# Optimization experiments

Measured on AMD Instinct MI355X. Metric: run time of the kernel, lower is better.

## Reference

```python
import jax, jax.numpy as jnp
import numpy as np

BATCH = 8192
IN_DIM = 2048
OUT_DIM = 2048
DEPTH = 5


def setup_inputs() -> dict:
    key = jax.random.key(0)
    k1, k2, k3, k4 = jax.random.split(key, 4)
    x = jax.random.normal(k1, (BATCH, IN_DIM), dtype=jnp.float32)
    hyperdimensional_weights = jax.random.normal(k2, (DEPTH, IN_DIM, OUT_DIM), dtype=jnp.float32)
    classical_weights = jax.random.normal(k3, (IN_DIM, OUT_DIM), dtype=jnp.float32)
    classical_biases = jax.random.normal(k4, (OUT_DIM,), dtype=jnp.float32)
    return {
        "x": x,
        "hyperdimensional_weights": hyperdimensional_weights,
        "classical_weights": classical_weights,
        "classical_biases": classical_biases,
    }


def _hyperdimensional_probs(hd_w):
    # angle = W[d, j, 0], phase = W[d, j, 1] for output index j (j < input_dims)
    depth, in_dim, _ = hd_w.shape
    angles = hd_w[:, :OUT_DIM, 0]   # [depth, out]
    phases = hd_w[:, :OUT_DIM, 1]   # [depth, out]
    # Initial uniform state 1/sqrt(n), replicated per output unit j.
    s0 = jnp.full((OUT_DIM, in_dim), 1.0 / np.sqrt(in_dim), dtype=jnp.complex64)

    def step(s, ang_ph):
        ang, ph = ang_ph                      # each [out]
        c = jnp.cos(ang)[:, None]
        sn = jnp.sin(ang)[:, None]
        # Circulant rotation: new[k] = cos*s[k] - sin*s[k+1] + sin*s[k-1] (cyclic)
        s = c * s - sn * jnp.roll(s, -1, axis=1) + sn * jnp.roll(s, 1, axis=1)
        # Global phase gate: diag(e^{i*phase})
        s = s * jnp.exp(1j * ph)[:, None]
        return s, None

    s, _ = jax.lax.scan(step, s0, (angles, phases))
    # probability = |state[0]|^2
    return jnp.abs(s[:, 0]) ** 2              # [out], real float32


def reference(x, hyperdimensional_weights, classical_weights, classical_biases):
    classical = x @ classical_weights + classical_biases            # [B, out]
    hd = _hyperdimensional_probs(hyperdimensional_weights)          # [out] (batch-independent)
    return jnp.tanh(classical + hd[None, :])
```

## Files before the change

kernel.cpp:

```cpp
#include <hip/hip_runtime.h>

#define BATCH 8192
#define DIM   2048
#define DEPTH 5


#define BUFSZ  65536
#define ABYTES 32768

typedef short bf16x8_t __attribute__((ext_vector_type(8)));
typedef float f32x4_t  __attribute__((ext_vector_type(4)));

__device__ __forceinline__ unsigned short f2bf(float f) {
  unsigned u = __float_as_uint(f);
  u += 0x7fffu + ((u >> 16) & 1u);
  return (unsigned short)(u >> 16);
}
__device__ __forceinline__ float bf2f(unsigned short h) {
  return __uint_as_float(((unsigned)h) << 16);
}

__global__ void prep_fused_kernel(const float* __restrict__ x,
                                  const float* __restrict__ hdw,
                                  const float* __restrict__ W,
                                  const float* __restrict__ bias,
                                  float* __restrict__ bias2,
                                  unsigned short* __restrict__ xhi,
                                  unsigned short* __restrict__ xlo,
                                  unsigned short* __restrict__ whi,
                                  unsigned short* __restrict__ wlo) {
  __shared__ float tile[32][33];
  const int b = blockIdx.x;
  const int tid = threadIdx.x;

  if (b < 8192) {
    size_t g = (size_t)b * 256 + tid;
    const float4* xp = (const float4*)(x + g * 8);
    float4 v0 = xp[0], v1 = xp[1];
    float v[8] = {v0.x, v0.y, v0.z, v0.w, v1.x, v1.y, v1.z, v1.w};
    bf16x8_t h, lo;
#pragma unroll
    for (int j = 0; j < 8; ++j) {
      unsigned short hj = f2bf(v[j]);
      h[j] = (short)hj;
      lo[j] = (short)f2bf(v[j] - bf2f(hj));
    }
    ((bf16x8_t*)xhi)[g] = h;
    ((bf16x8_t*)xlo)[g] = lo;
  } else if (b < 12288) {
    const int t = b - 8192;
    const int k0 = (t >> 6) * 32;
    const int n0 = (t & 63) * 32;
    const int tx = tid & 31;
    const int ty = tid >> 5;
#pragma unroll
    for (int r = 0; r < 32; r += 8)
      tile[ty + r][tx] = W[(size_t)(k0 + ty + r) * DIM + n0 + tx];
    __syncthreads();
    const int n = tid >> 3;
    const int kq = (tid & 7) * 4;
    ushort4 hv, lv;
    float vv0 = tile[kq + 0][n], vv1 = tile[kq + 1][n];
    float vv2 = tile[kq + 2][n], vv3 = tile[kq + 3][n];
    hv.x = f2bf(vv0); lv.x = f2bf(vv0 - bf2f(hv.x));
    hv.y = f2bf(vv1); lv.y = f2bf(vv1 - bf2f(hv.y));
    hv.z = f2bf(vv2); lv.z = f2bf(vv2 - bf2f(hv.z));
    hv.w = f2bf(vv3); lv.w = f2bf(vv3 - bf2f(hv.w));
    const size_t o = (size_t)(n0 + n) * DIM + k0 + kq;
    *(ushort4*)(whi + o) = hv;
    *(ushort4*)(wlo + o) = lv;
  } else {
    int j = (b - 12288) * 256 + tid;
    float p = 1.0f;
#pragma unroll
    for (int d = 0; d < DEPTH; ++d)
      p *= cosf(hdw[(size_t)d * DIM * DIM + (size_t)j * DIM]);
    bias2[j] = bias[j] + p * p * (1.0f / 2048.0f);
  }
}

#define GLDS(SRC, OFF)                                                         \
  __builtin_amdgcn_global_load_lds(                                            \
      (const __attribute__((address_space(1))) unsigned int*)(SRC),            \
      (__attribute__((address_space(3))) unsigned int*)(smem + (OFF)), 16, 0, 0)

#define MFMA16(A, B, C) __builtin_amdgcn_mfma_f32_16x16x32_bf16((A), (B), (C), 0, 0, 0)

#define STAGE(KO, SO)                                                          \
  do {                                                                         \
    GLDS(sAh + (KO),             (SO) + 0              + wdst);                \
    GLDS(sAh + 128 * DIM + (KO), (SO) + 8192           + wdst);                \
    GLDS(sAl + (KO),             (SO) + 16384          + wdst);                \
    GLDS(sAl + 128 * DIM + (KO), (SO) + 24576          + wdst);                \
    GLDS(sBh + (KO),             (SO) + ABYTES + 0     + wdst);                \
    GLDS(sBh + 128 * DIM + (KO), (SO) + ABYTES + 8192  + wdst);                \
    GLDS(sBl + (KO),             (SO) + ABYTES + 16384 + wdst);                \
    GLDS(sBl + 128 * DIM + (KO), (SO) + ABYTES + 24576 + wdst);                \
  } while (0)

#define READ_BQ(PB, NT, H0, L0, H1, L1)                                        \
  do {                                                                         \
    H0 = *(const bf16x8_t*)((PB) + (NT) * 1024);                               \
    L0 = *(const bf16x8_t*)((PB) + 16384 + (NT) * 1024);                       \
    H1 = *(const bf16x8_t*)((PB) + ((NT) + 1) * 1024);                         \
    L1 = *(const bf16x8_t*)((PB) + 16384 + ((NT) + 1) * 1024);                 \
  } while (0)

#define QMFMA(H0, L0, H1, L1, C0)                                              \
  do {                                                                         \
    __builtin_amdgcn_s_setprio(1);                                             \
    _Pragma("unroll")                                                          \
    for (int mt = 0; mt < 4; ++mt) {                                           \
      acc[mt][C0]     = MFMA16(A_h[mt], H0, acc[mt][C0]);                      \
      acc[mt][C0]     = MFMA16(A_h[mt], L0, acc[mt][C0]);                      \
      acc[mt][C0]     = MFMA16(A_l[mt], H0, acc[mt][C0]);                      \
      acc[mt][C0 + 1] = MFMA16(A_h[mt], H1, acc[mt][C0 + 1]);                  \
      acc[mt][C0 + 1] = MFMA16(A_h[mt], L1, acc[mt][C0 + 1]);                  \
      acc[mt][C0 + 1] = MFMA16(A_l[mt], H1, acc[mt][C0 + 1]);                  \
    }                                                                          \
    __builtin_amdgcn_s_setprio(0);                                             \
  } while (0)

__global__ __launch_bounds__(512, 2) void gemm_pipe_kernel(
    const unsigned short* __restrict__ Ah, const unsigned short* __restrict__ Al,
    const unsigned short* __restrict__ Bh, const unsigned short* __restrict__ Bl,
    const float* __restrict__ bias2, float* __restrict__ out) {
  __shared__ float4 smem4[2 * BUFSZ / 16];
  char* smem = (char*)smem4;

  const int tid  = threadIdx.x;
  const int lane = tid & 63;
  const int wave = tid >> 6;
  const int wm   = wave >> 1;
  const int wn   = wave & 1;
  const int l15  = lane & 15;
  const int kl   = lane >> 4;
  const int bm = blockIdx.x;
  const int bn = blockIdx.y;

  const int rsub = wave * 16 + (lane >> 2);
  const int kg   = ((lane & 3) ^ ((lane >> 3) & 3)) * 8;
  const unsigned short* sAh = Ah + ((size_t)(bm * 256 + rsub)) * DIM + kg;
  const unsigned short* sAl = Al + ((size_t)(bm * 256 + rsub)) * DIM + kg;
  const unsigned short* sBh = Bh + ((size_t)(bn * 256 + rsub)) * DIM + kg;
  const unsigned short* sBl = Bl + ((size_t)(bn * 256 + rsub)) * DIM + kg;
  const unsigned wdst = wave * 1024;

  const int foff = l15 * 64 + ((kl * 16) ^ (((l15 >> 1) & 3) << 4));

  const f32x4_t vzero = {0.f, 0.f, 0.f, 0.f};
  f32x4_t acc[4][8];
#pragma unroll
  for (int i = 0; i < 4; ++i)
#pragma unroll
    for (int j = 0; j < 8; ++j) acc[i][j] = vzero;

  bf16x8_t A_h[4], A_l[4];
  bf16x8_t Bc_h0, Bc_l0, Bc_h1, Bc_l1;
  bf16x8_t Bn_h0, Bn_l0, Bn_h1, Bn_l1;

  STAGE(0, 0);
  asm volatile("s_waitcnt vmcnt(0)" ::: "memory");
  asm volatile("s_barrier" ::: "memory");
  {
    const char* pA0 = smem + wm * 4096 + foff;
#pragma unroll
    for (int mt = 0; mt < 4; ++mt) {
      A_h[mt] = *(const bf16x8_t*)(pA0 + mt * 1024);
      A_l[mt] = *(const bf16x8_t*)(pA0 + 16384 + mt * 1024);
    }
    const char* pB0 = smem + ABYTES + wn * 8192 + foff;
    READ_BQ(pB0, 0, Bc_h0, Bc_l0, Bc_h1, Bc_l1);
  }

#pragma unroll 1
  for (int t = 0; t < 64; ++t) {
    const unsigned bo = (unsigned)(t & 1) * BUFSZ;
    const unsigned so = bo ^ BUFSZ;
    const char* pB = smem + bo + ABYTES + wn * 8192 + foff;

    if (t < 63) {
      const int ko = (t + 1) * 32;
      STAGE(ko, so);
    }

    READ_BQ(pB, 2, Bn_h0, Bn_l0, Bn_h1, Bn_l1);
    QMFMA(Bc_h0, Bc_l0, Bc_h1, Bc_l1, 0);

    READ_BQ(pB, 4, Bc_h0, Bc_l0, Bc_h1, Bc_l1);
    QMFMA(Bn_h0, Bn_l0, Bn_h1, Bn_l1, 2);

    READ_BQ(pB, 6, Bn_h0, Bn_l0, Bn_h1, Bn_l1);
    QMFMA(Bc_h0, Bc_l0, Bc_h1, Bc_l1, 4);

    asm volatile("s_waitcnt lgkmcnt(0)" ::: "memory");
    if (t < 63) { asm volatile("s_waitcnt vmcnt(0)" ::: "memory"); }
    asm volatile("s_barrier" ::: "memory");

    if (t < 63) {
      const char* pBn = smem + so + ABYTES + wn * 8192 + foff;
      READ_BQ(pBn, 0, Bc_h0, Bc_l0, Bc_h1, Bc_l1);
    }

    QMFMA(Bn_h0, Bn_l0, Bn_h1, Bn_l1, 6);

    if (t < 63) {
      const char* pAn = smem + so + wm * 4096 + foff;
#pragma unroll
      for (int mt = 0; mt < 4; ++mt) {
        A_h[mt] = *(const bf16x8_t*)(pAn + mt * 1024);
        A_l[mt] = *(const bf16x8_t*)(pAn + 16384 + mt * 1024);
      }
    }
  }

  const int orow0 = bm * 256 + wm * 64;
  const int ocol0 = bn * 256 + wn * 128;
#pragma unroll
  for (int nt = 0; nt < 8; ++nt) {
    const int col = ocol0 + nt * 16 + l15;
    const float b2 = bias2[col];
#pragma unroll
    for (int mt = 0; mt < 4; ++mt) {
      const int row = orow0 + mt * 16 + kl * 4;
#pragma unroll
      for (int r = 0; r < 4; ++r) {
        float z = acc[mt][nt][r] + b2;
        float e = __expf(2.0f * z);
        out[(size_t)(row + r) * DIM + col] = 1.0f - 2.0f / (e + 1.0f);
      }
    }
  }
}

extern "C" void kernel_launch(void* const* d_in, const int* in_sizes, int n_in,
                              void* d_out, int out_size, void* d_ws, size_t ws_size,
                              hipStream_t stream) {
  const float* x   = (const float*)d_in[0];
  const float* hdw = (const float*)d_in[1];
  const float* W   = (const float*)d_in[2];
  const float* b   = (const float*)d_in[3];
  float* out = (float*)d_out;

  char* ws = (char*)d_ws;
  unsigned short* xhi  = (unsigned short*)ws;
  unsigned short* xlo  = xhi + (size_t)BATCH * DIM;
  unsigned short* wThi = xlo + (size_t)BATCH * DIM;
  unsigned short* wTlo = wThi + (size_t)DIM * DIM;
  float*          bias2 = (float*)(wTlo + (size_t)DIM * DIM);

  prep_fused_kernel<<<12296, 256, 0, stream>>>(
      x, hdw, W, b, bias2, xhi, xlo, wThi, wTlo);
  gemm_pipe_kernel<<<dim3(BATCH / 256, DIM / 256), 512, 0, stream>>>(
      xhi, xlo, wThi, wTlo, bias2, out);
}
```

Baseline: 327.6 us.

## Fuse x bf16 hi/lo split into GEMM A-tile staging

Drops the separate pass that splits x into bf16 hi/lo arrays in workspace. The GEMM now loads fp32 x rows straight into registers, splits them in-kernel and writes the swizzled hi/lo tiles into LDS, overlapped with MFMA work. This removes the global write and re-read of the split x arrays. In exchange, each x tile is re-read and re-split by every N-block (8 times), and the kernel carries more VGPRs and VALU work inside the main loop.

```diff
diff --git a/kernel.cpp b/kernel.cpp
--- a/kernel.cpp
+++ b/kernel.cpp
@@ -20,35 +20,18 @@
   return __uint_as_float(((unsigned)h) << 16);
 }
 
-__global__ void prep_fused_kernel(const float* __restrict__ x,
-                                  const float* __restrict__ hdw,
+__global__ void prep_fused_kernel(const float* __restrict__ hdw,
                                   const float* __restrict__ W,
                                   const float* __restrict__ bias,
                                   float* __restrict__ bias2,
-                                  unsigned short* __restrict__ xhi,
-                                  unsigned short* __restrict__ xlo,
                                   unsigned short* __restrict__ whi,
                                   unsigned short* __restrict__ wlo) {
   __shared__ float tile[32][33];
   const int b = blockIdx.x;
   const int tid = threadIdx.x;
 
-  if (b < 8192) {
-    size_t g = (size_t)b * 256 + tid;
-    const float4* xp = (const float4*)(x + g * 8);
-    float4 v0 = xp[0], v1 = xp[1];
-    float v[8] = {v0.x, v0.y, v0.z, v0.w, v1.x, v1.y, v1.z, v1.w};
-    bf16x8_t h, lo;
-#pragma unroll
-    for (int j = 0; j < 8; ++j) {
-      unsigned short hj = f2bf(v[j]);
-      h[j] = (short)hj;
-      lo[j] = (short)f2bf(v[j] - bf2f(hj));
-    }
-    ((bf16x8_t*)xhi)[g] = h;
-    ((bf16x8_t*)xlo)[g] = lo;
-  } else if (b < 12288) {
-    const int t = b - 8192;
+  if (b < 4096) {
+    const int t = b;
     const int k0 = (t >> 6) * 32;
     const int n0 = (t & 63) * 32;
     const int tx = tid & 31;
@@ -70,7 +53,7 @@
     *(ushort4*)(whi + o) = hv;
     *(ushort4*)(wlo + o) = lv;
   } else {
-    int j = (b - 12288) * 256 + tid;
+    int j = (b - 4096) * 256 + tid;
     float p = 1.0f;
 #pragma unroll
     for (int d = 0; d < DEPTH; ++d)
@@ -86,16 +69,43 @@
 
 #define MFMA16(A, B, C) __builtin_amdgcn_mfma_f32_16x16x32_bf16((A), (B), (C), 0, 0, 0)
 
-#define STAGE(KO, SO)                                                          \
-  do {                                                                         \
-    GLDS(sAh + (KO),             (SO) + 0              + wdst);                \
-    GLDS(sAh + 128 * DIM + (KO), (SO) + 8192           + wdst);                \
-    GLDS(sAl + (KO),             (SO) + 16384          + wdst);                \
-    GLDS(sAl + 128 * DIM + (KO), (SO) + 24576          + wdst);                \
+#define STAGE_B(KO, SO)                                                        \
+  do {                                                                         \
     GLDS(sBh + (KO),             (SO) + ABYTES + 0     + wdst);                \
     GLDS(sBh + 128 * DIM + (KO), (SO) + ABYTES + 8192  + wdst);                \
     GLDS(sBl + (KO),             (SO) + ABYTES + 16384 + wdst);                \
     GLDS(sBl + 128 * DIM + (KO), (SO) + ABYTES + 24576 + wdst);                \
+  } while (0)
+
+#define ALOAD(KO)                                                              \
+  do {                                                                         \
+    xf0 = *(const float4*)(xsrc + (KO));                                       \
+    xf1 = *(const float4*)(xsrc + (KO) + 4);                                   \
+    xf2 = *(const float4*)(xsrc + (KO) + 8);                                   \
+    xf3 = *(const float4*)(xsrc + (KO) + 12);                                  \
+  } while (0)
+
+#define ASPLIT_WRITE(SO)                                                       \
+  do {                                                                         \
+    float f[16] = {xf0.x, xf0.y, xf0.z, xf0.w, xf1.x, xf1.y, xf1.z, xf1.w,     \
+                   xf2.x, xf2.y, xf2.z, xf2.w, xf3.x, xf3.y, xf3.z, xf3.w};    \
+    bf16x8_t h0, l0, h1, l1;                                                   \
+    _Pragma("unroll")                                                          \
+    for (int j = 0; j < 8; ++j) {                                              \
+      unsigned short hj = f2bf(f[j]);                                          \
+      h0[j] = (short)hj;                                                       \
+      l0[j] = (short)f2bf(f[j] - bf2f(hj));                                    \
+    }                                                                          \
+    _Pragma("unroll")                                                          \
+    for (int j = 0; j < 8; ++j) {                                              \
+      unsigned short hj = f2bf(f[8 + j]);                                      \
+      h1[j] = (short)hj;                                                       \
+      l1[j] = (short)f2bf(f[8 + j] - bf2f(hj));                                \
+    }                                                                          \
+    *(bf16x8_t*)(smem + (SO) + ad0)         = h0;                              \
+    *(bf16x8_t*)(smem + (SO) + ad0 + 16384) = l0;                              \
+    *(bf16x8_t*)(smem + (SO) + ad1)         = h1;                              \
+    *(bf16x8_t*)(smem + (SO) + ad1 + 16384) = l1;                              \
   } while (0)
 
 #define READ_BQ(PB, NT, H0, L0, H1, L1)                                        \
@@ -122,7 +132,7 @@
   } while (0)
 
 __global__ __launch_bounds__(512, 2) void gemm_pipe_kernel(
-    const unsigned short* __restrict__ Ah, const unsigned short* __restrict__ Al,
+    const float* __restrict__ X,
     const unsigned short* __restrict__ Bh, const unsigned short* __restrict__ Bl,
     const float* __restrict__ bias2, float* __restrict__ out) {
   __shared__ float4 smem4[2 * BUFSZ / 16];
@@ -140,12 +150,18 @@
 
   const int rsub = wave * 16 + (lane >> 2);
   const int kg   = ((lane & 3) ^ ((lane >> 3) & 3)) * 8;
-  const unsigned short* sAh = Ah + ((size_t)(bm * 256 + rsub)) * DIM + kg;
-  const unsigned short* sAl = Al + ((size_t)(bm * 256 + rsub)) * DIM + kg;
   const unsigned short* sBh = Bh + ((size_t)(bn * 256 + rsub)) * DIM + kg;
   const unsigned short* sBl = Bl + ((size_t)(bn * 256 + rsub)) * DIM + kg;
   const unsigned wdst = wave * 1024;
 
+  const int row_local = wave * 32 + (lane >> 1);
+  const int khalf     = lane & 1;
+  const int sA        = (lane >> 2) & 3;
+  const float* xsrc = X + (size_t)(bm * 256 + row_local) * DIM + khalf * 16;
+  const int ad0 = row_local * 64 + (((khalf * 2 + 0) ^ sA) * 16);
+  const int ad1 = row_local * 64 + (((khalf * 2 + 1) ^ sA) * 16);
+  float4 xf0, xf1, xf2, xf3;
+
   const int foff = l15 * 64 + ((kl * 16) ^ (((l15 >> 1) & 3) << 4));
 
   const f32x4_t vzero = {0.f, 0.f, 0.f, 0.f};
@@ -159,8 +175,10 @@
   bf16x8_t Bc_h0, Bc_l0, Bc_h1, Bc_l1;
   bf16x8_t Bn_h0, Bn_l0, Bn_h1, Bn_l1;
 
-  STAGE(0, 0);
-  asm volatile("s_waitcnt vmcnt(0)" ::: "memory");
+  ALOAD(0);
+  STAGE_B(0, 0);
+  ASPLIT_WRITE(0);
+  asm volatile("s_waitcnt vmcnt(0) lgkmcnt(0)" ::: "memory");
   asm volatile("s_barrier" ::: "memory");
   {
     const char* pA0 = smem + wm * 4096 + foff;
@@ -181,7 +199,8 @@
 
     if (t < 63) {
       const int ko = (t + 1) * 32;
-      STAGE(ko, so);
+      ALOAD(ko);
+      STAGE_B(ko, so);
     }
 
     READ_BQ(pB, 2, Bn_h0, Bn_l0, Bn_h1, Bn_l1);
@@ -189,6 +208,8 @@
 
     READ_BQ(pB, 4, Bc_h0, Bc_l0, Bc_h1, Bc_l1);
     QMFMA(Bn_h0, Bn_l0, Bn_h1, Bn_l1, 2);
+
+    if (t < 63) { ASPLIT_WRITE(so); }
 
     READ_BQ(pB, 6, Bn_h0, Bn_l0, Bn_h1, Bn_l1);
     QMFMA(Bc_h0, Bc_l0, Bc_h1, Bc_l1, 4);
@@ -243,14 +264,11 @@
   float* out = (float*)d_out;
 
   char* ws = (char*)d_ws;
-  unsigned short* xhi  = (unsigned short*)ws;
-  unsigned short* xlo  = xhi + (size_t)BATCH * DIM;
-  unsigned short* wThi = xlo + (size_t)BATCH * DIM;
+  unsigned short* wThi = (unsigned short*)ws;
   unsigned short* wTlo = wThi + (size_t)DIM * DIM;
   float*          bias2 = (float*)(wTlo + (size_t)DIM * DIM);
 
-  prep_fused_kernel<<<12296, 256, 0, stream>>>(
-      x, hdw, W, b, bias2, xhi, xlo, wThi, wTlo);
+  prep_fused_kernel<<<4104, 256, 0, stream>>>(hdw, W, b, bias2, wThi, wTlo);
   gemm_pipe_kernel<<<dim3(BATCH / 256, DIM / 256), 512, 0, stream>>>(
-      xhi, xlo, wThi, wTlo, bias2, out);
-}
+      x, wThi, wTlo, bias2, out);
+}
```

New measurement: 351.3 us. 7.2% more time.
